# Kernel tuning notes

Hardware: AMD Instinct MI355X
Metric: run time of the kernel (lower is better)

Reference implementation:

```python
import jax, jax.numpy as jnp
import numpy as np

THRESHOLD = 0.5  # classification_threshold from __init__


def setup_inputs() -> dict:
    key = jax.random.key(0)
    x = jax.random.uniform(key, (4096, 8192), dtype=jnp.float32)  # [B, S]
    return {"x": x}


def reference(x) -> jnp.ndarray:
    # tf.scan without initializer: out[0] = row[0]; then
    # out[t] = x[t] * (1 - (out[t-1] > thr) * (x[t] > thr)).
    # Init carry = -inf so the first step's (a > thr) is False -> out[0] = x[0].
    thr = jnp.asarray(THRESHOLD, x.dtype)

    def step(a, t):  # a, t: [B]
        keep = 1.0 - (a > thr).astype(t.dtype) * (t > thr).astype(t.dtype)
        out = t * keep
        return out, out

    init = jnp.full((x.shape[0],), -jnp.inf, dtype=x.dtype)
    _, ys = jax.lax.scan(step, init, jnp.swapaxes(x, 0, 1))  # scan over seq axis
    return jnp.swapaxes(ys, 0, 1)  # [B, S]
```

## Files before the change

kernel.cpp:

```cpp
#include <hip/hip_runtime.h>


constexpr int S = 8192;
constexpr int TPB = 1024;
constexpr int EPT = S / TPB;
constexpr float THR = 0.5f;

__global__ __launch_bounds__(TPB) void notwo_kernel(const float* __restrict__ x,
                                                    float* __restrict__ out) {
    const int row = blockIdx.x;
    const int tid = threadIdx.x;
    const size_t rowoff = (size_t)row * S;

    const float4* xv = reinterpret_cast<const float4*>(x + rowoff) + tid * 2;
    float4 v0 = xv[0];
    float4 v1 = xv[1];
    float f[EPT] = {v0.x, v0.y, v0.z, v0.w, v1.x, v1.y, v1.z, v1.w};

    const int base = tid * EPT;

    int lastz = -1;
    #pragma unroll
    for (int k = 0; k < EPT; ++k) {
        if (!(f[k] > THR)) lastz = base + k;
    }

    const int lane = tid & 63;
    const int wv = tid >> 6;
    int incl = lastz;
    #pragma unroll
    for (int off = 1; off < 64; off <<= 1) {
        int up = __shfl_up(incl, off, 64);
        incl = max(incl, up);
    }
    __shared__ int wtot[TPB / 64];
    if (lane == 63) wtot[wv] = incl;
    __syncthreads();
    int prefix = -1;
    #pragma unroll
    for (int w = 0; w < TPB / 64; ++w) {
        int t = wtot[w];
        if (w < wv) prefix = max(prefix, t);
    }
    int up1 = __shfl_up(incl, 1, 64);
    int excl = (lane == 0) ? -1 : up1;
    int carry = max(prefix, excl);

    #pragma unroll
    for (int k = 0; k < EPT; ++k) {
        const int t = base + k;
        const bool c = f[k] > THR;
        if (c && (((t - carry) & 1) == 0)) f[k] = 0.0f;
        if (!c) carry = t;
    }

    float4* ov = reinterpret_cast<float4*>(out + rowoff) + tid * 2;
    ov[0] = make_float4(f[0], f[1], f[2], f[3]);
    ov[1] = make_float4(f[4], f[5], f[6], f[7]);
}

extern "C" void kernel_launch(void* const* d_in, const int* in_sizes, int n_in,
                              void* d_out, int out_size, void* d_ws, size_t ws_size,
                              hipStream_t stream) {
    const float* x = (const float*)d_in[0];
    float* out = (float*)d_out;
    const int B = out_size / S;
    notwo_kernel<<<B, TPB, 0, stream>>>(x, out);
}
```

Baseline: 46.50 us.

## Interleave per-wave row segments so each load instruction is fully coalesced

Each wave now owns a contiguous 512-float segment split into two 256-float halves. Each lane loads one float4 from each half, so every wave-wide load covers a contiguous 1KB span, where before each lane loaded two adjacent float4s with a 32-byte lane stride. The lane scan now runs two independent max-scans, one per half, and chains the carry from the first half into the second. This aims to make the memory accesses better coalesced, at the cost of extra shuffles for the doubled scan.

```diff
diff --git a/kernel.cpp b/kernel.cpp
--- a/kernel.cpp
+++ b/kernel.cpp
@@ -1,62 +1,84 @@
 #include <hip/hip_runtime.h>
 
 
+typedef float floatx4 __attribute__((ext_vector_type(4)));
+
 constexpr int S = 8192;
 constexpr int TPB = 1024;
-constexpr int EPT = S / TPB;
+constexpr int WAVES = TPB / 64;
+constexpr int WFLOATS = S / WAVES;
 constexpr float THR = 0.5f;
 
 __global__ __launch_bounds__(TPB) void notwo_kernel(const float* __restrict__ x,
                                                     float* __restrict__ out) {
     const int row = blockIdx.x;
     const int tid = threadIdx.x;
-    const size_t rowoff = (size_t)row * S;
-
-    const float4* xv = reinterpret_cast<const float4*>(x + rowoff) + tid * 2;
-    float4 v0 = xv[0];
-    float4 v1 = xv[1];
-    float f[EPT] = {v0.x, v0.y, v0.z, v0.w, v1.x, v1.y, v1.z, v1.w};
-
-    const int base = tid * EPT;
-
-    int lastz = -1;
-    #pragma unroll
-    for (int k = 0; k < EPT; ++k) {
-        if (!(f[k] > THR)) lastz = base + k;
-    }
-
     const int lane = tid & 63;
     const int wv = tid >> 6;
-    int incl = lastz;
+    const size_t rowoff = (size_t)row * S;
+    const size_t wbase = rowoff + (size_t)wv * WFLOATS;
+
+    const int baseA = wv * WFLOATS + lane * 4;
+    const int baseB = baseA + 256;
+
+    floatx4 a = *reinterpret_cast<const floatx4*>(x + wbase + lane * 4);
+    floatx4 b = *reinterpret_cast<const floatx4*>(x + wbase + 256 + lane * 4);
+    float fa[4] = {a.x, a.y, a.z, a.w};
+    float fb[4] = {b.x, b.y, b.z, b.w};
+
+    int lzA = -1, lzB = -1;
+    #pragma unroll
+    for (int k = 0; k < 4; ++k) { if (!(fa[k] > THR)) lzA = baseA + k; }
+    #pragma unroll
+    for (int k = 0; k < 4; ++k) { if (!(fb[k] > THR)) lzB = baseB + k; }
+
+    int inclA = lzA, inclB = lzB;
     #pragma unroll
     for (int off = 1; off < 64; off <<= 1) {
-        int up = __shfl_up(incl, off, 64);
-        incl = max(incl, up);
+        int uA = __shfl_up(inclA, off, 64);
+        int uB = __shfl_up(inclB, off, 64);
+        inclA = max(inclA, uA);
+        inclB = max(inclB, uB);
     }
-    __shared__ int wtot[TPB / 64];
-    if (lane == 63) wtot[wv] = incl;
+    const int waveAmax = __shfl(inclA, 63, 64);
+    const int waveBmax = __shfl(inclB, 63, 64);
+
+    __shared__ int wtot[WAVES];
+    if (lane == 0) wtot[wv] = max(waveAmax, waveBmax);
     __syncthreads();
     int prefix = -1;
     #pragma unroll
-    for (int w = 0; w < TPB / 64; ++w) {
+    for (int w = 0; w < WAVES; ++w) {
         int t = wtot[w];
         if (w < wv) prefix = max(prefix, t);
     }
-    int up1 = __shfl_up(incl, 1, 64);
-    int excl = (lane == 0) ? -1 : up1;
-    int carry = max(prefix, excl);
+
+    int upA = __shfl_up(inclA, 1, 64);
+    int upB = __shfl_up(inclB, 1, 64);
+    int exclA = (lane == 0) ? -1 : upA;
+    int exclB = (lane == 0) ? -1 : upB;
+    int carryA = max(prefix, exclA);
+    int carryB = max(max(prefix, waveAmax), exclB);
 
     #pragma unroll
-    for (int k = 0; k < EPT; ++k) {
-        const int t = base + k;
-        const bool c = f[k] > THR;
-        if (c && (((t - carry) & 1) == 0)) f[k] = 0.0f;
-        if (!c) carry = t;
+    for (int k = 0; k < 4; ++k) {
+        const int t = baseA + k;
+        const bool c = fa[k] > THR;
+        if (c && (((t - carryA) & 1) == 0)) fa[k] = 0.0f;
+        if (!c) carryA = t;
+    }
+    #pragma unroll
+    for (int k = 0; k < 4; ++k) {
+        const int t = baseB + k;
+        const bool c = fb[k] > THR;
+        if (c && (((t - carryB) & 1) == 0)) fb[k] = 0.0f;
+        if (!c) carryB = t;
     }
 
-    float4* ov = reinterpret_cast<float4*>(out + rowoff) + tid * 2;
-    ov[0] = make_float4(f[0], f[1], f[2], f[3]);
-    ov[1] = make_float4(f[4], f[5], f[6], f[7]);
+    floatx4 oa = {fa[0], fa[1], fa[2], fa[3]};
+    floatx4 ob = {fb[0], fb[1], fb[2], fb[3]};
+    *reinterpret_cast<floatx4*>(out + wbase + lane * 4) = oa;
+    *reinterpret_cast<floatx4*>(out + wbase + 256 + lane * 4) = ob;
 }
 
 extern "C" void kernel_launch(void* const* d_in, const int* in_sizes, int n_in,
```

Result: faster. 44.27 us (-4.8%).
